# Optimization experiments

Measured on AMD Instinct MI355X. Metric: run time of the kernel, lower is better.

The kernel has to match this reference:

```python
import jax, jax.numpy as jnp
import numpy as np

L, H, N, F, E, FF, OUT, B = 4, 8, 1024, 128, 128, 512, 64, 32


def setup_inputs() -> dict:
    key = jax.random.key(0)
    ks = jax.random.split(key, 16)
    s = 0.02
    return {
        "x": jax.random.normal(ks[0], (B, N, F), jnp.float32),
        "adj": jax.random.randint(ks[1], (N, N), 0, 2, jnp.int32),
        "Ws": jax.random.normal(ks[2], (L, H, E, F), jnp.float32) * s,
        "bs": jnp.zeros((L, H, E), jnp.float32),
        "As": jax.random.normal(ks[3], (L, H, 2 * E, N), jnp.float32) * s,
        "W1": jax.random.normal(ks[4], (L, FF, F), jnp.float32) * s,
        "b1": jnp.zeros((L, FF), jnp.float32),
        "W2": jax.random.normal(ks[5], (L, F, FF), jnp.float32) * s,
        "b2": jnp.zeros((L, F), jnp.float32),
        "g1": jnp.ones((L, F), jnp.float32),
        "be1": jnp.zeros((L, F), jnp.float32),
        "g2": jnp.ones((L, F), jnp.float32),
        "be2": jnp.zeros((L, F), jnp.float32),
        "Wo": jax.random.normal(ks[6], (OUT, N * F), jnp.float32) * s,
        "bo": jnp.zeros((OUT,), jnp.float32),
    }


def _ln(x, g, b, eps=1e-5):
    m = jnp.mean(x, axis=-1, keepdims=True)
    v = jnp.mean((x - m) ** 2, axis=-1, keepdims=True)
    return (x - m) / jnp.sqrt(v + eps) * g + b


def reference(x, adj, Ws, bs, As, W1, b1, W2, b2, g1, be1, g2, be2, Wo, bo):
    # mask[j, i] = 1 if j is a neighbor of i (adj_matrix[:, i] > 0 in torch source)
    mask = (adj > 0).astype(x.dtype)
    E_ = Ws.shape[2]
    for l in range(Ws.shape[0]):
        # per-head projection: h [B, H, N, E]
        h = jnp.einsum('bnf,hef->bhne', x, Ws[l]) + bs[l][None, :, None, :]
        # score[b,h,i] = h_i . a[:E, i] + (sum_{j in N(i)} h_j) . a[E:, i]
        s1 = jnp.einsum('bhne,hen->bhn', h, As[l][:, :E_, :])
        hn = jnp.einsum('jn,bhje->bhne', mask, h)  # neighbor sums
        s2 = jnp.einsum('bhne,hen->bhn', hn, As[l][:, E_:, :])
        score = s1 + s2  # [B, H, N]
        # attention row i is the constant score[b,h,i] broadcast over columns,
        # so attention @ h == score[...,None] * h.sum(over nodes)
        hsum = h.sum(axis=2)  # [B, H, E]
        hp = score[..., None] * hsum[:, :, None, :]  # [B, H, N, E]
        att = jax.nn.leaky_relu(hp, 0.01).sum(axis=1)  # sum over heads -> [B, N, F]
        x = _ln(x + att, g1[l], be1[l])
        ff = jax.nn.relu(x @ W1[l].T + b1[l]) @ W2[l].T + b2[l]
        x = _ln(x + ff, g2[l], be2[l])
    flat = x.reshape(x.shape[0], -1)  # [B, N*F]
    return jax.nn.relu(flat) @ Wo.T + bo
```

## Files before the change

### kernel.cpp

```cpp
#include <hip/hip_runtime.h>

#define L_ 4
#define H_ 8
#define Nn 1024
#define F_ 128
#define E_ 128
#define FF_ 512
#define OUT_ 64
#define B_ 32
#define KTOT (Nn * F_)

typedef unsigned short u16;
typedef __bf16 bf16_t;
typedef __attribute__((ext_vector_type(8))) __bf16 bf16x8;
typedef __attribute__((ext_vector_type(4))) float f32x4;

__device__ __forceinline__ u16 f2b(float v) {
    bf16_t h = (bf16_t)v;
    return __builtin_bit_cast(u16, h);
}

typedef const __attribute__((address_space(1))) void* gvp;
typedef __attribute__((address_space(3))) void* lvp;
__device__ __forceinline__ void gll16(const void* g, void* l) {
    __builtin_amdgcn_global_load_lds((gvp)g, (lvp)l, 16, 0, 0);
}

template <int R>
__device__ __forceinline__ void stage(const u16* __restrict__ g, int ldg,
                                      u16* lds, int w, int l) {
    const int r8 = l >> 3, jq = l & 7;
#pragma unroll
    for (int i = 0; i < R / 32; ++i) {
        const int row0 = w * (R / 4) + i * 8;
        const int row = row0 + r8;
        gll16(g + (long)row * ldg + ((jq ^ (row & 7)) << 3), lds + row0 * 64);
    }
}

template <int BM, int BN, bool DUAL, int EPI, int BSH, bool GSWAP, bool DBUF>
__global__ __launch_bounds__(256) void k_mfma(
    const u16* __restrict__ A, int lda, long sAz,
    const u16* __restrict__ Bhp, const u16* __restrict__ Blp, int ldb, long sBz,
    const float* __restrict__ bias,
    float* __restrict__ Cf, u16* __restrict__ Cb, int ldc, long sCz, int K)
{
    constexpr int WN = (BN == 64) ? 1 : ((BM == 64) ? 4 : 2);
    constexpr int WM = 4 / WN;
    constexpr int SM = BM / WM, SN = BN / WN;
    constexpr int MF = SM / 16, NF = SN / 16;
    constexpr int BUFE = BM * 64 + (DUAL ? 2 : 1) * BN * 64;
    __shared__ __align__(16) u16 lds[BUFE * (DBUF ? 2 : 1)];
    const int t = threadIdx.x;
    const int w = t >> 6, l = t & 63, lr = l & 15, lg = l >> 4;
    const int wm0 = (w / WN) * SM, wn0 = (w % WN) * SN;
    const int bidm = GSWAP ? blockIdx.z : blockIdx.x;
    const int bidz = GSWAP ? blockIdx.x : blockIdx.z;
    const int m0 = bidm * BM, n0 = blockIdx.y * BN;
    A += BSH ? ((long)(bidz >> 1) * sAz + (long)(bidz & 1) * 128)
             : (long)bidz * sAz;
    Bhp += (long)(bidz >> BSH) * sBz;
    if (DUAL) Blp += (long)bidz * sBz;

    f32x4 acc[MF][NF] = {};

    auto stageAll = [&](u16* base, int k0) {
        stage<BM>(A + (long)m0 * lda + k0, lda, base, w, l);
        stage<BN>(Bhp + (long)n0 * ldb + k0, ldb, base + BM * 64, w, l);
        if (DUAL) stage<BN>(Blp + (long)n0 * ldb + k0, ldb, base + BM * 64 + BN * 64, w, l);
    };
    auto compute = [&](const u16* base) {
        const u16* Al = base;
        const u16* Bh = base + BM * 64;
        const u16* Bl = Bh + BN * 64;
#pragma unroll
        for (int ks = 0; ks < 2; ++ks) {
            bf16x8 af[MF], bh[NF], bl[NF];
            const int kq = ks * 4 + lg;
#pragma unroll
            for (int mf = 0; mf < MF; ++mf) {
                int row = wm0 + mf * 16 + lr;
                af[mf] = *reinterpret_cast<const bf16x8*>(&Al[row * 64 + ((kq ^ (row & 7)) << 3)]);
            }
#pragma unroll
            for (int nf = 0; nf < NF; ++nf) {
                int row = wn0 + nf * 16 + lr;
                int off = row * 64 + ((kq ^ (row & 7)) << 3);
                bh[nf] = *reinterpret_cast<const bf16x8*>(&Bh[off]);
                if (DUAL) bl[nf] = *reinterpret_cast<const bf16x8*>(&Bl[off]);
            }
#pragma unroll
            for (int mf = 0; mf < MF; ++mf)
#pragma unroll
                for (int nf = 0; nf < NF; ++nf) {
                    acc[mf][nf] = __builtin_amdgcn_mfma_f32_16x16x32_bf16(af[mf], bh[nf], acc[mf][nf], 0, 0, 0);
                    if (DUAL)
                        acc[mf][nf] = __builtin_amdgcn_mfma_f32_16x16x32_bf16(af[mf], bl[nf], acc[mf][nf], 0, 0, 0);
                }
        }
    };

    if (DBUF) {
        stageAll(lds, 0);
        __syncthreads();
        int cur = 0;
        for (int k0 = 0; k0 < K; k0 += 64) {
            if (k0 + 64 < K) stageAll(lds + (cur ^ 1) * BUFE, k0 + 64);
            compute(lds + cur * BUFE);
            __syncthreads();
            cur ^= 1;
        }
    } else {
        for (int k0 = 0; k0 < K; k0 += 64) {
            __syncthreads();
            stageAll(lds, k0);
            __syncthreads();
            compute(lds);
        }
    }

    float bv[NF];
    if (EPI) {
#pragma unroll
        for (int nf = 0; nf < NF; ++nf) bv[nf] = bias[n0 + wn0 + nf * 16 + lr];
    }
    if (EPI == 1) Cb += (long)bidz * sCz;
    else          Cf += (long)bidz * sCz;
#pragma unroll
    for (int mf = 0; mf < MF; ++mf)
#pragma unroll
        for (int nf = 0; nf < NF; ++nf)
#pragma unroll
            for (int r = 0; r < 4; ++r) {
                long row = m0 + wm0 + mf * 16 + lg * 4 + r;
                int col = n0 + wn0 + nf * 16 + lr;
                float v = acc[mf][nf][r];
                if (EPI) v += bv[nf];
                if (EPI == 1) Cb[row * ldc + col] = f2b(fmaxf(v, 0.f));
                else          Cf[row * ldc + col] = v;
            }
}

template <bool LAST>
__global__ __launch_bounds__(256) void k_ff2_ln2(
    const u16* __restrict__ Tb,
    const u16* __restrict__ W2b,
    const float* __restrict__ b2,
    float* __restrict__ xc,
    const float* __restrict__ g, const float* __restrict__ be,
    u16* __restrict__ xh, u16* __restrict__ xl,
    float* __restrict__ xsp,
    u16* __restrict__ xrb)
{
    __shared__ __align__(16) char uu[49152];
    const int t = threadIdx.x;
    const int w = t >> 6, l = t & 63, lr = l & 15, lg = l >> 4;
    const int wn0 = w * 32;
    const int m0 = blockIdx.x * 64;
    f32x4 acc[4][2] = {};

    auto stageAll = [&](char* base, int k0) {
        stage<64>(Tb + (long)m0 * FF_ + k0, FF_, (u16*)base, w, l);
        stage<128>(W2b + k0, FF_, (u16*)(base + 8192), w, l);
    };
    auto compute = [&](const char* base) {
        const u16* Al = (const u16*)base;
        const u16* Bh = (const u16*)(base + 8192);
#pragma unroll
        for (int ks = 0; ks < 2; ++ks) {
            const int kq = ks * 4 + lg;
            bf16x8 af[4], bfr[2];
#pragma unroll
            for (int mf = 0; mf < 4; ++mf) {
                int row = mf * 16 + lr;
                af[mf] = *reinterpret_cast<const bf16x8*>(&Al[row * 64 + ((kq ^ (row & 7)) << 3)]);
            }
#pragma unroll
            for (int nf = 0; nf < 2; ++nf) {
                int row = wn0 + nf * 16 + lr;
                bfr[nf] = *reinterpret_cast<const bf16x8*>(&Bh[row * 64 + ((kq ^ (row & 7)) << 3)]);
            }
#pragma unroll
            for (int mf = 0; mf < 4; ++mf)
#pragma unroll
                for (int nf = 0; nf < 2; ++nf)
                    acc[mf][nf] = __builtin_amdgcn_mfma_f32_16x16x32_bf16(af[mf], bfr[nf], acc[mf][nf], 0, 0, 0);
        }
    };

    stageAll(uu, 0);
    __syncthreads();
    int cur = 0;
    for (int k0 = 0; k0 < FF_; k0 += 64) {
        if (k0 + 64 < FF_) stageAll(uu + (cur ^ 1) * 24576, k0 + 64);
        compute(uu + cur * 24576);
        __syncthreads();
        cur ^= 1;
    }
    float (*buf)[133] = (float(*)[133])uu;
    float (*ps)[128]  = (float(*)[128])(uu + 36864);
    float bv[2] = { b2[wn0 + lr], b2[wn0 + 16 + lr] };
#pragma unroll
    for (int mf = 0; mf < 4; ++mf)
#pragma unroll
        for (int nf = 0; nf < 2; ++nf)
#pragma unroll
            for (int r = 0; r < 4; ++r)
                buf[mf * 16 + lg * 4 + r][wn0 + nf * 16 + lr] = acc[mf][nf][r] + bv[nf];
    __syncthreads();
    const float gl0 = g[l], gl1 = g[l + 64], bl0 = be[l], bl1 = be[l + 64];
    float s0 = 0.f, s1 = 0.f;
#pragma unroll
    for (int rr = 0; rr < 16; ++rr) {
        const int row = w * 16 + rr;
        const long xb_ = (long)(m0 + row) * F_;
        float v0 = buf[row][l] + xc[xb_ + l];
        float v1 = buf[row][l + 64] + xc[xb_ + l + 64];
        float sum = v0 + v1;
#pragma unroll
        for (int o = 32; o; o >>= 1) sum += __shfl_xor(sum, o);
        const float mean = sum * (1.f / 128.f);
        const float d0 = v0 - mean, d1 = v1 - mean;
        float vs = d0 * d0 + d1 * d1;
#pragma unroll
        for (int o = 32; o; o >>= 1) vs += __shfl_xor(vs, o);
        const float rstd = rsqrtf(vs * (1.f / 128.f) + 1e-5f);
        float o0 = d0 * rstd * gl0 + bl0;
        float o1 = d1 * rstd * gl1 + bl1;
        if (LAST) {
            xrb[xb_ + l] = f2b(fmaxf(o0, 0.f));
            xrb[xb_ + l + 64] = f2b(fmaxf(o1, 0.f));
        } else {
            xc[xb_ + l] = o0;       xc[xb_ + l + 64] = o1;
            buf[row][l] = o0;       buf[row][l + 64] = o1;
            s0 += o0;               s1 += o1;
        }
    }
    if (!LAST) {
        ps[w][l] = s0; ps[w][l + 64] = s1;
        __syncthreads();
        const int b = m0 >> 10, nb0 = m0 & 1023, seg = (m0 >> 6) & 15;
        const int n8 = (t & 7) * 8, fb = t >> 3;
#pragma unroll
        for (int i = 0; i < 4; ++i) {
            const int f = fb + 32 * i;
            union { u16 u[8]; float4 v; } Hv, Lv;
#pragma unroll
            for (int j = 0; j < 8; ++j) {
                float v = buf[n8 + j][f];
                bf16_t h = (bf16_t)v;
                Hv.u[j] = __builtin_bit_cast(u16, h);
                Lv.u[j] = f2b(v - (float)h);
            }
            const long ob = ((long)b * F_ + f) * Nn + nb0 + n8;
            *reinterpret_cast<float4*>(&xh[ob]) = Hv.v;
            *reinterpret_cast<float4*>(&xl[ob]) = Lv.v;
        }
        if (t < 128)
            xsp[((long)b * 16 + seg) * 128 + t] =
                ps[0][t] + ps[1][t] + ps[2][t] + ps[3][t];
    }
}

__global__ __launch_bounds__(256) void k_final_mfma(
    const u16* __restrict__ xrb, const u16* __restrict__ Wob,
    float* __restrict__ part)
{
    __shared__ __align__(16) u16 Al[32 * 512];
    const int c = blockIdx.x;
    const long k0 = (long)c * 512;
    const int t = threadIdx.x, w = t >> 6, l = t & 63, lr = l & 15, lg = l >> 4;
#pragma unroll
    for (int i = 0; i < 8; ++i) {
        int ch = i * 256 + t, row = ch >> 6, jq = ch & 63;
        *reinterpret_cast<float4*>(&Al[row * 512 + ((jq ^ (row & 7)) << 3)]) =
            *reinterpret_cast<const float4*>(&xrb[(long)row * KTOT + k0 + (jq << 3)]);
    }
    __syncthreads();
    f32x4 acc[2] = {};
    const u16* Bp = Wob + (long)(w * 16 + lr) * KTOT + k0 + lg * 8;
#pragma unroll
    for (int ks = 0; ks < 16; ++ks) {
        bf16x8 bfr = *reinterpret_cast<const bf16x8*>(Bp + ks * 32);
        const int j8 = ks * 4 + lg;
#pragma unroll
        for (int mf = 0; mf < 2; ++mf) {
            int row = mf * 16 + lr;
            bf16x8 af = *reinterpret_cast<const bf16x8*>(&Al[row * 512 + ((j8 ^ (row & 7)) << 3)]);
            acc[mf] = __builtin_amdgcn_mfma_f32_16x16x32_bf16(af, bfr, acc[mf], 0, 0, 0);
        }
    }
#pragma unroll
    for (int mf = 0; mf < 2; ++mf)
#pragma unroll
        for (int r = 0; r < 4; ++r) {
            int b = mf * 16 + lg * 4 + r, o = w * 16 + lr;
            part[((long)c * B_ + b) * OUT_ + o] = acc[mf][r];
        }
}

__global__ void k_final_reduce(const float* __restrict__ part,
                               const float* __restrict__ bo, float* __restrict__ out)
{
    int i = blockIdx.x * 256 + threadIdx.x;
    int o = i & 63;
    float s = bo[o];
    for (int c = 0; c < 256; ++c) s += part[(long)c * (B_ * OUT_) + i];
    out[i] = s;
}

__global__ __launch_bounds__(256) void k_maskT(const int* __restrict__ adj,
                                               u16* __restrict__ maskTb,
                                               int* __restrict__ degi)
{
    __shared__ u16 tl[64][65];
    const int j0 = blockIdx.x * 64, n0 = blockIdx.y * 64, t = threadIdx.x;
#pragma unroll
    for (int i = 0; i < 16; ++i) {
        int s = i * 256 + t, jl = s >> 6, nl = s & 63;
        tl[jl][nl] = (adj[(long)(j0 + jl) * Nn + n0 + nl] > 0) ? 0x3F80 : 0;
    }
    __syncthreads();
    if (t < 64) {
        int c = 0;
#pragma unroll
        for (int jl = 0; jl < 64; ++jl) c += (tl[jl][t] != 0);
        atomicAdd(&degi[n0 + t], c);
    }
#pragma unroll
    for (int i = 0; i < 16; ++i) {
        int s = i * 256 + t, nl = s >> 6, jl = s & 63;
        maskTb[(long)(n0 + nl) * Nn + j0 + jl] = tl[jl][nl];
    }
}

__global__ __launch_bounds__(256) void k_tpb(const float* __restrict__ in,
                                             u16* __restrict__ out, int R, int C)
{
    __shared__ float tl[64][65];
    const int c0 = blockIdx.x * 64, r0 = blockIdx.y * 64, t = threadIdx.x;
    in  += (long)blockIdx.z * R * C;
    out += (long)blockIdx.z * R * C;
#pragma unroll
    for (int i = 0; i < 16; ++i) {
        int s = i * 256 + t, rl = s >> 6, cl = s & 63;
        tl[rl][cl] = in[(long)(r0 + rl) * C + c0 + cl];
    }
    __syncthreads();
#pragma unroll
    for (int i = 0; i < 16; ++i) {
        int s = i * 256 + t, cl = s >> 6, rl = s & 63;
        out[(long)(c0 + cl) * R + r0 + rl] = f2b(tl[rl][cl]);
    }
}

__global__ void k_cvtW(const float* __restrict__ W1, const float* __restrict__ W2,
                       u16* __restrict__ W1b, u16* __restrict__ W2b)
{
    int i = blockIdx.x * 256 + threadIdx.x;
    W1b[i] = f2b(W1[i]);
    W2b[i] = f2b(W2[i]);
}

__global__ void k_cvtWo(const float* __restrict__ Wo, u16* __restrict__ Wob)
{
    long i = ((long)blockIdx.x * 256 + threadIdx.x) * 8;
    float4 a = *reinterpret_cast<const float4*>(&Wo[i]);
    float4 b = *reinterpret_cast<const float4*>(&Wo[i + 4]);
    union { u16 u[8]; float4 v; } r;
    r.u[0] = f2b(a.x); r.u[1] = f2b(a.y); r.u[2] = f2b(a.z); r.u[3] = f2b(a.w);
    r.u[4] = f2b(b.x); r.u[5] = f2b(b.y); r.u[6] = f2b(b.z); r.u[7] = f2b(b.w);
    *reinterpret_cast<float4*>(&Wob[i]) = r.v;
}

__global__ __launch_bounds__(256) void k_xpose(const float* __restrict__ x,
                                               u16* __restrict__ xh, u16* __restrict__ xl)
{
    __shared__ float tile[64][132];
    const int b = blockIdx.y, n0 = blockIdx.x * 64, t = threadIdx.x;
#pragma unroll
    for (int i = 0; i < 8; ++i) {
        int s = i * 256 + t, nl = s >> 5, f4 = (s & 31) << 2;
        float4 v = *reinterpret_cast<const float4*>(&x[((long)b * Nn + n0 + nl) * F_ + f4]);
        tile[nl][f4] = v.x; tile[nl][f4 + 1] = v.y;
        tile[nl][f4 + 2] = v.z; tile[nl][f4 + 3] = v.w;
    }
    __syncthreads();
    const int f = t >> 1, nb = (t & 1) << 5;
    const long ob = ((long)b * F_ + f) * Nn + n0 + nb;
    union { u16 u[8]; float4 v; } Hv, Lv;
#pragma unroll
    for (int i = 0; i < 32; i += 8) {
#pragma unroll
        for (int j = 0; j < 8; ++j) {
            float v = tile[nb + i + j][f];
            bf16_t h = (bf16_t)v;
            Hv.u[j] = __builtin_bit_cast(u16, h);
            Lv.u[j] = f2b(v - (float)h);
        }
        *reinterpret_cast<float4*>(&xh[ob + i]) = Hv.v;
        *reinterpret_cast<float4*>(&xl[ob + i]) = Lv.v;
    }
}

__global__ __launch_bounds__(256) void k_xs2(const float* __restrict__ x, float* __restrict__ xsp)
{
    __shared__ float sh[2][128];
    const int seg = blockIdx.x, b = blockIdx.y, t = threadIdx.x;
    const int f = t & 127, h2 = t >> 7;
    const float* p = x + ((long)b * Nn + seg * 64 + h2 * 32) * F_ + f;
    float s = 0.f;
    for (int i = 0; i < 32; ++i) s += p[(long)i * F_];
    sh[h2][f] = s;
    __syncthreads();
    if (t < 128) xsp[((long)b * 16 + seg) * 128 + t] = sh[0][t] + sh[1][t];
}

__global__ void k_hsum(const float* __restrict__ xsp, const float* __restrict__ Wl,
                       const float* __restrict__ bsl, float* __restrict__ hsum)
{
    __shared__ float xs[128];
    const int i = blockIdx.x * 256 + threadIdx.x;
    const int b = i >> 10;
    if (threadIdx.x < 128) {
        const float* xp = xsp + (long)b * 16 * 128 + threadIdx.x;
        float v = 0.f;
#pragma unroll
        for (int sg = 0; sg < 16; ++sg) v += xp[sg * 128];
        xs[threadIdx.x] = v;
    }
    __syncthreads();
    const int e = i & 127, h = (i >> 7) & 7;
    const float* w = Wl + ((long)h * E_ + e) * F_;
    float s = 0.f;
    for (int f = 0; f < F_; ++f) s += xs[f] * w[f];
    hsum[i] = s + (float)Nn * bsl[h * E_ + e];
}

__global__ void k_d12(const float* __restrict__ As, const float* __restrict__ bs,
                      float* __restrict__ d12all)
{
    const int lyr = blockIdx.y;
    const float* Asl = As + (long)lyr * H_ * 2 * E_ * Nn;
    const float* bsl = bs + (long)lyr * H_ * E_;
    int i = blockIdx.x * 256 + threadIdx.x;
    int n = i & 1023, h = (i >> 10) & 7, w = i >> 13;
    const float* a = Asl + ((long)h * 2 * E_ + (long)w * E_) * Nn + n;
    const float* bb = bsl + h * E_;
    float s = 0.f;
    for (int e = 0; e < E_; ++e) s += bb[e] * a[(long)e * Nn];
    d12all[(long)lyr * 2 * H_ * Nn + ((long)w * H_ + h) * Nn + n] = s;
}

__global__ __launch_bounds__(256) void k_score_ln1(
    float* __restrict__ x, const float* __restrict__ y,
    const float* __restrict__ Ct, const float* __restrict__ d12,
    const int* __restrict__ degi, const float* __restrict__ hsum,
    const float* __restrict__ g, const float* __restrict__ be,
    u16* __restrict__ xb)
{
    const int n = blockIdx.x, t = threadIdx.x;
    __shared__ float c1[H_][128], c2[H_][128];
    __shared__ float sbs[H_];
#pragma unroll
    for (int i = 0; i < 4; ++i) {
        int s = i * 256 + t, h = s >> 7, f = s & 127;
        c1[h][f] = Ct[((long)(2 * h) * Nn + n) * F_ + f];
        c2[h][f] = Ct[((long)(2 * h + 1) * Nn + n) * F_ + f];
    }
    if (t < H_) sbs[t] = d12[(long)t * Nn + n] + (float)degi[n] * d12[(long)(H_ + t) * Nn + n];
    __syncthreads();
    const int w = t >> 6, l = t & 63;
    const float gl0 = g[l], gl1 = g[l + 64], bl0 = be[l], bl1 = be[l + 64];
    for (int bi = 0; bi < 8; ++bi) {
        const int b = w * 8 + bi;
        const long base = ((long)b * Nn + n) * F_;
        float x0 = x[base + l], x1 = x[base + l + 64];
        float y0 = y[base + l], y1 = y[base + l + 64];
        float a0 = 0.f, a1 = 0.f;
#pragma unroll
        for (int h = 0; h < H_; ++h) {
            float p = x0 * c1[h][l] + x1 * c1[h][l + 64]
                    + y0 * c2[h][l] + y1 * c2[h][l + 64];
#pragma unroll
            for (int o = 32; o; o >>= 1) p += __shfl_xor(p, o);
            float s = p + sbs[h];
            float h0 = hsum[((long)b * H_ + h) * E_ + l];
            float h1 = hsum[((long)b * H_ + h) * E_ + l + 64];
            float p0 = s * h0, p1 = s * h1;
            a0 += (p0 > 0.f ? p0 : 0.01f * p0);
            a1 += (p1 > 0.f ? p1 : 0.01f * p1);
        }
        float v0 = x0 + a0, v1 = x1 + a1;
        float sum = v0 + v1;
#pragma unroll
        for (int o = 32; o; o >>= 1) sum += __shfl_xor(sum, o);
        const float mean = sum * (1.f / 128.f);
        const float d0 = v0 - mean, d1 = v1 - mean;
        float vs = d0 * d0 + d1 * d1;
#pragma unroll
        for (int o = 32; o; o >>= 1) vs += __shfl_xor(vs, o);
        const float rstd = rsqrtf(vs * (1.f / 128.f) + 1e-5f);
        float o0 = d0 * rstd * gl0 + bl0;
        float o1 = d1 * rstd * gl1 + bl1;
        x[base + l] = o0;        x[base + l + 64] = o1;
        xb[base + l] = f2b(o0);  xb[base + l + 64] = f2b(o1);
    }
}

extern "C" void kernel_launch(void* const* d_in, const int* in_sizes, int n_in,
                              void* d_out, int out_size, void* d_ws, size_t ws_size,
                              hipStream_t stream)
{
    const float* x_in = (const float*)d_in[0];
    const int*   adj  = (const int*)d_in[1];
    const float* Ws   = (const float*)d_in[2];
    const float* bs   = (const float*)d_in[3];
    const float* As   = (const float*)d_in[4];
    const float* W1   = (const float*)d_in[5];
    const float* b1   = (const float*)d_in[6];
    const float* W2   = (const float*)d_in[7];
    const float* b2   = (const float*)d_in[8];
    const float* g1   = (const float*)d_in[9];
    const float* be1  = (const float*)d_in[10];
    const float* g2   = (const float*)d_in[11];
    const float* be2  = (const float*)d_in[12];
    const float* Wo   = (const float*)d_in[13];
    const float* bo   = (const float*)d_in[14];
    float* out = (float*)d_out;

    char* wsb = (char*)d_ws;
    u16*   maskTb = (u16*)wsb;
    float* xc     = (float*)(wsb + (2L << 20));
    float* y      = (float*)(wsb + (18L << 20));
    u16*   Tb     = (u16*)(wsb + (34L << 20));
    float* CtAll  = (float*)(wsb + (66L << 20));
    u16*   xb     = (u16*)(wsb + (98L << 20));
    u16*   xrb    = (u16*)(wsb + (106L << 20));
    u16*   Wob    = (u16*)(wsb + (114L << 20));
    float* part   = (float*)(wsb + (130L << 20));
    u16*   xTh    = (u16*)(wsb + (132L << 20));
    u16*   xTl    = (u16*)(wsb + (140L << 20));
    u16*   AsTb   = (u16*)(wsb + (148L << 20));
    u16*   WsTb   = (u16*)(wsb + (164L << 20));
    char*  S      = wsb + (166L << 20);
    int*   degi   = (int*)S;
    float* xsp    = (float*)(S + (4L << 10));
    float* hsum   = (float*)(S + (260L << 10));
    float* d12all = (float*)(S + (388L << 10));
    u16*   W1b    = (u16*)(S + (644L << 10));
    u16*   W2b    = (u16*)(S + (1156L << 10));

    hipMemsetAsync(degi, 0, Nn * sizeof(int), stream);
    hipMemcpyAsync(xc, x_in, sizeof(float) * (long)B_ * Nn * F_,
                   hipMemcpyDeviceToDevice, stream);
    k_maskT<<<dim3(16, 16), 256, 0, stream>>>(adj, maskTb, degi);
    k_cvtW<<<(L_ * FF_ * F_) / 256, 256, 0, stream>>>(W1, W2, W1b, W2b);
    k_cvtWo<<<(OUT_ * KTOT) / (256 * 8), 256, 0, stream>>>(Wo, Wob);
    k_tpb<<<dim3(16, 4, L_ * H_), 256, 0, stream>>>(As, AsTb, 2 * E_, Nn);
    k_tpb<<<dim3(2, 2, L_ * H_), 256, 0, stream>>>(Ws, WsTb, E_, F_);
    k_xpose<<<dim3(16, B_), 256, 0, stream>>>(x_in, xTh, xTl);
    k_xs2<<<dim3(16, B_), 256, 0, stream>>>(x_in, xsp);
    k_d12<<<dim3((2 * H_ * Nn) / 256, L_), 256, 0, stream>>>(As, bs, d12all);
    k_mfma<64, 128, false, 0, 1, false, false><<<dim3(16, 1, 64), 256, 0, stream>>>(
        AsTb, 2 * E_, (long)Nn * 2 * E_, WsTb, nullptr, E_, (long)F_ * E_,
        nullptr, CtAll, nullptr, F_, (long)Nn * F_, E_);

    for (int l = 0; l < L_; ++l) {
        const float* Wl  = Ws + (long)l * H_ * E_ * F_;
        const float* bsl = bs + (long)l * H_ * E_;

        k_mfma<128, 64, true, 0, 0, true, true><<<dim3(32, 2, 8), 256, 0, stream>>>(
            maskTb, Nn, 0L, xTh, xTl, Nn, (long)F_ * Nn,
            nullptr, y, nullptr, F_, (long)Nn * F_, Nn);

        k_hsum<<<(B_ * H_ * E_) / 256, 256, 0, stream>>>(xsp, Wl, bsl, hsum);
        k_score_ln1<<<Nn, 256, 0, stream>>>(
            xc, y, CtAll + (long)l * 16 * Nn * F_, d12all + (long)l * 2 * H_ * Nn,
            degi, hsum, g1 + l * F_, be1 + l * F_, xb);
        k_mfma<128, 128, false, 1, 0, false, false><<<dim3(256, 4), 256, 0, stream>>>(
            xb, F_, 0L, W1b + (long)l * FF_ * F_, nullptr, F_, 0L,
            b1 + l * FF_, nullptr, Tb, FF_, 0L, F_);
        if (l < L_ - 1)
            k_ff2_ln2<false><<<512, 256, 0, stream>>>(
                Tb, W2b + (long)l * F_ * FF_, b2 + l * F_, xc,
                g2 + l * F_, be2 + l * F_, xTh, xTl, xsp, nullptr);
        else
            k_ff2_ln2<true><<<512, 256, 0, stream>>>(
                Tb, W2b + (long)l * F_ * FF_, b2 + l * F_, xc,
                g2 + l * F_, be2 + l * F_, nullptr, nullptr, nullptr, xrb);
    }

    k_final_mfma<<<256, 256, 0, stream>>>(xrb, Wob, part);
    k_final_reduce<<<(B_ * OUT_) / 256, 256, 0, stream>>>(part, bo, out);
}
```

Before: 416.6 us.

## Fuse FF1 GEMM into FF2+LN2 kernel, keeping hidden activations in LDS

Merges the first feed-forward GEMM (x@W1+b1, ReLU) into the second GEMM and layernorm kernel. Each 64-row block computes its hidden activations one 128-column chunk at a time and writes them to swizzled LDS as bf16, then consumes them right away for the W2 product. This removes the global round trip of the 32768x512 bf16 intermediate and one kernel launch per layer. In exchange it drops the double-buffered pipelining, adds extra syncthreads per chunk, and makes every block restage the W1 and W2 weights, which may lower overlap.

```diff
diff --git a/kernel.cpp b/kernel.cpp
--- a/kernel.cpp
+++ b/kernel.cpp
@@ -142,8 +142,10 @@
 }
 
 template <bool LAST>
-__global__ __launch_bounds__(256) void k_ff2_ln2(
-    const u16* __restrict__ Tb,
+__global__ __launch_bounds__(256) void k_ff_ln2(
+    const u16* __restrict__ xb,
+    const u16* __restrict__ W1b,
+    const float* __restrict__ b1,
     const u16* __restrict__ W2b,
     const float* __restrict__ b2,
     float* __restrict__ xc,
@@ -152,53 +154,96 @@
     float* __restrict__ xsp,
     u16* __restrict__ xrb)
 {
-    __shared__ __align__(16) char uu[49152];
+    __shared__ __align__(16) u16 lds[32768];
     const int t = threadIdx.x;
     const int w = t >> 6, l = t & 63, lr = l & 15, lg = l >> 4;
     const int wn0 = w * 32;
     const int m0 = blockIdx.x * 64;
-    f32x4 acc[4][2] = {};
-
-    auto stageAll = [&](char* base, int k0) {
-        stage<64>(Tb + (long)m0 * FF_ + k0, FF_, (u16*)base, w, l);
-        stage<128>(W2b + k0, FF_, (u16*)(base + 8192), w, l);
-    };
-    auto compute = [&](const char* base) {
-        const u16* Al = (const u16*)base;
-        const u16* Bh = (const u16*)(base + 8192);
-#pragma unroll
-        for (int ks = 0; ks < 2; ++ks) {
-            const int kq = ks * 4 + lg;
-            bf16x8 af[4], bfr[2];
-#pragma unroll
-            for (int mf = 0; mf < 4; ++mf) {
-                int row = mf * 16 + lr;
-                af[mf] = *reinterpret_cast<const bf16x8*>(&Al[row * 64 + ((kq ^ (row & 7)) << 3)]);
+    u16* A0 = lds;
+    u16* P0 = lds + 8192;
+    u16* W0 = lds + 16384;
+
+    stage<64>(xb + (long)m0 * F_,      F_, A0, w, l);
+    stage<64>(xb + (long)m0 * F_ + 64, F_, A0 + 4096, w, l);
+
+    f32x4 acc2[4][2] = {};
+    for (int c = 0; c < 4; ++c) {
+        __syncthreads();
+        stage<128>(W1b + (long)(c * 128) * F_,      F_, W0, w, l);
+        stage<128>(W1b + (long)(c * 128) * F_ + 64, F_, W0 + 8192, w, l);
+        __syncthreads();
+        f32x4 acc1[4][2] = {};
+#pragma unroll
+        for (int kh = 0; kh < 2; ++kh) {
+            const u16* Ah = A0 + kh * 4096;
+            const u16* Wh = W0 + kh * 8192;
+#pragma unroll
+            for (int ks = 0; ks < 2; ++ks) {
+                const int kq = ks * 4 + lg;
+                bf16x8 af[4], bfr[2];
+#pragma unroll
+                for (int mf = 0; mf < 4; ++mf) {
+                    int row = mf * 16 + lr;
+                    af[mf] = *reinterpret_cast<const bf16x8*>(&Ah[row * 64 + ((kq ^ (row & 7)) << 3)]);
+                }
+#pragma unroll
+                for (int nf = 0; nf < 2; ++nf) {
+                    int row = wn0 + nf * 16 + lr;
+                    bfr[nf] = *reinterpret_cast<const bf16x8*>(&Wh[row * 64 + ((kq ^ (row & 7)) << 3)]);
+                }
+#pragma unroll
+                for (int mf = 0; mf < 4; ++mf)
+#pragma unroll
+                    for (int nf = 0; nf < 2; ++nf)
+                        acc1[mf][nf] = __builtin_amdgcn_mfma_f32_16x16x32_bf16(af[mf], bfr[nf], acc1[mf][nf], 0, 0, 0);
             }
-#pragma unroll
-            for (int nf = 0; nf < 2; ++nf) {
-                int row = wn0 + nf * 16 + lr;
-                bfr[nf] = *reinterpret_cast<const bf16x8*>(&Bh[row * 64 + ((kq ^ (row & 7)) << 3)]);
+        }
+        float b1v[2] = { b1[c * 128 + wn0 + lr], b1[c * 128 + wn0 + 16 + lr] };
+#pragma unroll
+        for (int mf = 0; mf < 4; ++mf)
+#pragma unroll
+            for (int nf = 0; nf < 2; ++nf)
+#pragma unroll
+                for (int r = 0; r < 4; ++r) {
+                    int row = mf * 16 + lg * 4 + r;
+                    int cc = wn0 + nf * 16 + lr;
+                    int c6 = cc & 63;
+                    float v = fmaxf(acc1[mf][nf][r] + b1v[nf], 0.f);
+                    P0[(cc >> 6) * 4096 + row * 64 + ((((c6 >> 3) ^ (row & 7))) << 3) + (c6 & 7)] = f2b(v);
+                }
+        __syncthreads();
+        stage<128>(W2b + c * 128,      FF_, W0, w, l);
+        stage<128>(W2b + c * 128 + 64, FF_, W0 + 8192, w, l);
+        __syncthreads();
+#pragma unroll
+        for (int kh = 0; kh < 2; ++kh) {
+            const u16* Ph = P0 + kh * 4096;
+            const u16* Wh = W0 + kh * 8192;
+#pragma unroll
+            for (int ks = 0; ks < 2; ++ks) {
+                const int kq = ks * 4 + lg;
+                bf16x8 af[4], bfr[2];
+#pragma unroll
+                for (int mf = 0; mf < 4; ++mf) {
+                    int row = mf * 16 + lr;
+                    af[mf] = *reinterpret_cast<const bf16x8*>(&Ph[row * 64 + ((kq ^ (row & 7)) << 3)]);
+                }
+#pragma unroll
+                for (int nf = 0; nf < 2; ++nf) {
+                    int row = wn0 + nf * 16 + lr;
+                    bfr[nf] = *reinterpret_cast<const bf16x8*>(&Wh[row * 64 + ((kq ^ (row & 7)) << 3)]);
+                }
+#pragma unroll
+                for (int mf = 0; mf < 4; ++mf)
+#pragma unroll
+                    for (int nf = 0; nf < 2; ++nf)
+                        acc2[mf][nf] = __builtin_amdgcn_mfma_f32_16x16x32_bf16(af[mf], bfr[nf], acc2[mf][nf], 0, 0, 0);
             }
-#pragma unroll
-            for (int mf = 0; mf < 4; ++mf)
-#pragma unroll
-                for (int nf = 0; nf < 2; ++nf)
-                    acc[mf][nf] = __builtin_amdgcn_mfma_f32_16x16x32_bf16(af[mf], bfr[nf], acc[mf][nf], 0, 0, 0);
-        }
-    };
-
-    stageAll(uu, 0);
-    __syncthreads();
-    int cur = 0;
-    for (int k0 = 0; k0 < FF_; k0 += 64) {
-        if (k0 + 64 < FF_) stageAll(uu + (cur ^ 1) * 24576, k0 + 64);
-        compute(uu + cur * 24576);
-        __syncthreads();
-        cur ^= 1;
-    }
-    float (*buf)[133] = (float(*)[133])uu;
-    float (*ps)[128]  = (float(*)[128])(uu + 36864);
+        }
+    }
+    __syncthreads();
+    float (*buf)[132] = (float(*)[132])lds;
+    float (*ps)[128]  = (float(*)[128])((char*)lds + 34816);
     float bv[2] = { b2[wn0 + lr], b2[wn0 + 16 + lr] };
 #pragma unroll
     for (int mf = 0; mf < 4; ++mf)
@@ -206,7 +251,7 @@
         for (int nf = 0; nf < 2; ++nf)
 #pragma unroll
             for (int r = 0; r < 4; ++r)
-                buf[mf * 16 + lg * 4 + r][wn0 + nf * 16 + lr] = acc[mf][nf][r] + bv[nf];
+                buf[mf * 16 + lg * 4 + r][wn0 + nf * 16 + lr] = acc2[mf][nf][r] + bv[nf];
     __syncthreads();
     const float gl0 = g[l], gl1 = g[l + 64], bl0 = be[l], bl1 = be[l + 64];
     float s0 = 0.f, s1 = 0.f;
@@ -533,7 +578,6 @@
     u16*   maskTb = (u16*)wsb;
     float* xc     = (float*)(wsb + (2L << 20));
     float* y      = (float*)(wsb + (18L << 20));
-    u16*   Tb     = (u16*)(wsb + (34L << 20));
     float* CtAll  = (float*)(wsb + (66L << 20));
     u16*   xb     = (u16*)(wsb + (98L << 20));
     u16*   xrb    = (u16*)(wsb + (106L << 20));
@@ -578,16 +622,15 @@
         k_score_ln1<<<Nn, 256, 0, stream>>>(
             xc, y, CtAll + (long)l * 16 * Nn * F_, d12all + (long)l * 2 * H_ * Nn,
             degi, hsum, g1 + l * F_, be1 + l * F_, xb);
-        k_mfma<128, 128, false, 1, 0, false, false><<<dim3(256, 4), 256, 0, stream>>>(
-            xb, F_, 0L, W1b + (long)l * FF_ * F_, nullptr, F_, 0L,
-            b1 + l * FF_, nullptr, Tb, FF_, 0L, F_);
         if (l < L_ - 1)
-            k_ff2_ln2<false><<<512, 256, 0, stream>>>(
-                Tb, W2b + (long)l * F_ * FF_, b2 + l * F_, xc,
+            k_ff_ln2<false><<<512, 256, 0, stream>>>(
+                xb, W1b + (long)l * FF_ * F_, b1 + l * FF_,
+                W2b + (long)l * F_ * FF_, b2 + l * F_, xc,
                 g2 + l * F_, be2 + l * F_, xTh, xTl, xsp, nullptr);
         else
-            k_ff2_ln2<true><<<512, 256, 0, stream>>>(
-                Tb, W2b + (long)l * F_ * FF_, b2 + l * F_, xc,
+            k_ff_ln2<true><<<512, 256, 0, stream>>>(
+                xb, W1b + (long)l * FF_ * F_, b1 + l * FF_,
+                W2b + (long)l * F_ * FF_, b2 + l * F_, xc,
                 g2 + l * F_, be2 + l * F_, nullptr, nullptr, nullptr, xrb);
     }
 
```

Result: faster. 394.2 us (-5.4%).
